# Optimization experiments

Hardware: AMD Instinct MI355X
Metric: run time of the kernel (lower is better)

Reference implementation:

```python
import jax, jax.numpy as jnp
import numpy as np

N_NODES = 50000
N_EDGES = 800000
N_FEAT = 128
N_HID = 256
N_PAIRS = 100000


def _gcn_norm(edge_index, n_nodes):
    # add self loops, compute D^-1/2 (A+I) D^-1/2 edge weights (PyG gcn_norm)
    loops = jnp.arange(n_nodes, dtype=edge_index.dtype)
    row = jnp.concatenate([edge_index[0], loops])
    col = jnp.concatenate([edge_index[1], loops])
    deg = jax.ops.segment_sum(jnp.ones_like(col, dtype=jnp.float32), col,
                              num_segments=n_nodes)
    dinv = jnp.where(deg > 0, jax.lax.rsqrt(deg), 0.0)
    norm = dinv[row] * dinv[col]  # [E + N]
    return row, col, norm


def _gcn_conv(x, W, b, row, col, norm, n_nodes):
    h = x @ W                       # [N, out]
    msg = h[row] * norm[:, None]    # gather + scale  [E+N, out]
    agg = jax.ops.segment_sum(msg, col, num_segments=n_nodes)  # scatter-add
    return agg + b


def setup_inputs() -> dict:
    key = jax.random.key(0)
    ks = jax.random.split(key, 9)
    edge_index = jax.random.randint(ks[0], (2, N_EDGES), 0, N_NODES, dtype=jnp.int64)
    features = jax.random.normal(ks[1], (N_NODES, N_FEAT), dtype=jnp.float32)
    mask = jax.random.randint(ks[2], (N_PAIRS, 2), 0, N_NODES, dtype=jnp.int64)
    s1 = 1.0 / np.sqrt(N_FEAT)
    s2 = 1.0 / np.sqrt(N_HID)
    W1 = jax.random.uniform(ks[3], (N_FEAT, N_HID), jnp.float32, -s1, s1)
    b1 = jnp.zeros((N_HID,), jnp.float32)
    W2 = jax.random.uniform(ks[4], (N_HID, N_FEAT), jnp.float32, -s2, s2)
    b2 = jnp.zeros((N_FEAT,), jnp.float32)
    Wl = jax.random.uniform(ks[5], (N_HID, 1), jnp.float32, -s2, s2)
    bl = jax.random.uniform(ks[6], (1,), jnp.float32, -s2, s2)
    return {"edge_index": edge_index, "features": features, "mask": mask,
            "W1": W1, "b1": b1, "W2": W2, "b2": b2, "Wl": Wl, "bl": bl}


def reference(edge_index, features, mask, W1, b1, W2, b2, Wl, bl):
    n = features.shape[0]
    row, col, norm = _gcn_norm(edge_index, n)
    h = _gcn_conv(features, W1, b1, row, col, norm, n)   # GCNConv a
    h = jax.nn.relu(h)                                   # dropout p=0 -> identity
    h = _gcn_conv(h, W2, b2, row, col, norm, n)          # GCNConv b
    mt = mask.T
    p1 = jax.lax.stop_gradient(h[mt[0]])                 # .detach()
    p2 = jax.lax.stop_gradient(h[mt[1]])
    hp = jnp.concatenate([p1, p2], axis=1)               # [n_pairs, 2*n_feat]
    return jax.nn.sigmoid(hp @ Wl + bl)
```

## Files before the change

### kernel.cpp

```cpp
#include <hip/hip_runtime.h>
#include <math.h>

#define NFEAT 128
#define NHID 256
#define NBLK 128

typedef __attribute__((ext_vector_type(8))) short short8;
typedef __attribute__((ext_vector_type(4))) float f32x4;

__device__ inline unsigned short f2bf(float f) {
  unsigned u = __float_as_uint(f);
  u += 0x7fffu + ((u >> 16) & 1u);
  return (unsigned short)(u >> 16);
}
__device__ inline float bflo(unsigned u) { return __uint_as_float(u << 16); }
__device__ inline float bfhi(unsigned u) { return __uint_as_float(u & 0xffff0000u); }


__device__ inline void packOne(const float* __restrict__ W,
                               unsigned short* __restrict__ Wp, int idx, int KS,
                               int OUT) {
  int lane = idx & 63;
  int t = idx >> 6;
  int ks = t % KS;
  int nt = t / KS;
  int n = nt * 16 + (lane & 15);
  int k0 = ks * 32 + (lane >> 4) * 8;
  unsigned short v[8];
#pragma unroll
  for (int j = 0; j < 8; j++) v[j] = f2bf(W[(size_t)(k0 + j) * OUT + n]);
  *reinterpret_cast<short8*>(Wp + (size_t)idx * 8) =
      *reinterpret_cast<short8*>(v);
}

__global__ __launch_bounds__(1024) void k_hist_pack(
    const int* __restrict__ col, int* __restrict__ hist2d, int nE, int nb,
    const float* __restrict__ W1, const float* __restrict__ W2,
    unsigned short* __restrict__ W1p, unsigned short* __restrict__ W2p) {
  if (blockIdx.x >= NBLK) {
    int idx = (blockIdx.x - NBLK) * 1024 + threadIdx.x;
    if (idx < 4096) packOne(W1, W1p, idx, 4, 256);
    else packOne(W2, W2p, idx - 4096, 8, 128);
    return;
  }
  __shared__ int h[1024];
  for (int i = threadIdx.x; i < nb; i += 1024) h[i] = 0;
  __syncthreads();
  int chunk = (nE + NBLK - 1) / NBLK;
  int beg = blockIdx.x * chunk, end = min(beg + chunk, nE);
  for (int e = beg + threadIdx.x; e < end; e += 1024)
    atomicAdd(&h[col[e] >> 6], 1);
  __syncthreads();
  for (int i = threadIdx.x; i < nb; i += 1024)
    hist2d[i * NBLK + blockIdx.x] = h[i];
}

__global__ __launch_bounds__(256) void k_bsum(const int* __restrict__ a,
                                              int* __restrict__ psum, int S,
                                              const float* __restrict__ b2,
                                              const float* __restrict__ Wl,
                                              const float* __restrict__ bl,
                                              float* __restrict__ Cbuf) {
  int t = threadIdx.x;
  if (blockIdx.x == gridDim.x - 1) {
    float v = (t < 128) ? b2[t] * (Wl[t] + Wl[128 + t]) : 0.f;
#pragma unroll
    for (int o = 32; o; o >>= 1) v += __shfl_down(v, o);
    __shared__ float fw[4];
    if ((t & 63) == 0) fw[t >> 6] = v;
    __syncthreads();
    if (t == 0) Cbuf[0] = fw[0] + fw[1] + fw[2] + fw[3] + bl[0];
    return;
  }
  int i = blockIdx.x * 256 + t;
  int v = (i < S) ? a[i] : 0;
#pragma unroll
  for (int o = 32; o; o >>= 1) v += __shfl_down(v, o);
  __shared__ int ws[4];
  if ((t & 63) == 0) ws[t >> 6] = v;
  __syncthreads();
  if (t == 0) psum[blockIdx.x] = ws[0] + ws[1] + ws[2] + ws[3];
}

__global__ __launch_bounds__(256) void k_s3m(const int* __restrict__ a,
                                             const int* __restrict__ psum,
                                             int* __restrict__ out, int S) {
  __shared__ int sh[256];
  __shared__ int ws[4];
  int t = threadIdx.x;
  int b = blockIdx.x;
  int partial = 0;
  for (int i = t; i < b; i += 256) partial += psum[i];
#pragma unroll
  for (int o = 32; o; o >>= 1) partial += __shfl_down(partial, o);
  if ((t & 63) == 0) ws[t >> 6] = partial;
  int i = b * 256 + t;
  int d = (i < S) ? a[i] : 0;
  sh[t] = d;
  __syncthreads();
  int base = ws[0] + ws[1] + ws[2] + ws[3];
  for (int o = 1; o < 256; o <<= 1) {
    int u = (t >= o) ? sh[t - o] : 0;
    __syncthreads();
    sh[t] += u;
    __syncthreads();
  }
  if (i < S) out[i] = base + sh[t] - d;
}

__global__ __launch_bounds__(1024) void k_part2(const int* __restrict__ row,
                                                const int* __restrict__ col,
                                                const int* __restrict__ sbase,
                                                unsigned* __restrict__ tmp,
                                                int nE, int nb) {
  __shared__ int cur[1024];
  for (int i = threadIdx.x; i < nb; i += 1024)
    cur[i] = sbase[i * NBLK + blockIdx.x];
  __syncthreads();
  int chunk = (nE + NBLK - 1) / NBLK;
  int beg = blockIdx.x * chunk, end = min(beg + chunk, nE);
  for (int e = beg + threadIdx.x; e < end; e += 1024) {
    int c = col[e];
    int pos = atomicAdd(&cur[c >> 6], 1);
    tmp[pos] = ((unsigned)(c & 63) << 16) | (unsigned)row[e];
  }
}

__global__ __launch_bounds__(256) void k_bsort_cvt(
    const unsigned* __restrict__ tmp, const int* __restrict__ sbase,
    int* __restrict__ ebuf, int* __restrict__ offs, float* __restrict__ dinv,
    const float* __restrict__ feat, unsigned short* __restrict__ xs, int n,
    int nE, int nb) {
  __shared__ int bins[64], cur[64];
  __shared__ float sdinv[64];
  int b = blockIdx.x;
  int beg = sbase[b * NBLK];
  int end = (b == nb - 1) ? nE : sbase[(b + 1) * NBLK];
  int t = threadIdx.x;
  if (t == 0 && b == nb - 1) offs[n] = nE;
  if (t < 64) bins[t] = 0;
  __syncthreads();
  for (int i = beg + t; i < end; i += 256) atomicAdd(&bins[tmp[i] >> 16], 1);
  __syncthreads();
  if (t < 64) {
    int v = bins[t];
    int s = v;
#pragma unroll
    for (int o = 1; o < 64; o <<= 1) {
      int u = __shfl_up(s, o);
      if (t >= o) s += u;
    }
    int off = beg + s - v;
    cur[t] = off;
    float dv = rsqrtf((float)(v + 1));
    sdinv[t] = dv;
    int node = b * 64 + t;
    if (node < n) {
      offs[node] = off;
      dinv[node] = dv;
    }
  }
  __syncthreads();
  for (int i = beg + t; i < end; i += 256) {
    unsigned p = tmp[i];
    int pos = atomicAdd(&cur[p >> 16], 1);
    ebuf[pos] = (int)(p & 0xffffu);
  }
  for (int i = t; i < 64 * 32; i += 256) {
    int r = i >> 5;
    int node = b * 64 + r;
    if (node >= n) break;
    float d = sdinv[r];
    float4 v = reinterpret_cast<const float4*>(feat)[(size_t)node * 32 + (i & 31)];
    unsigned short o[4] = {f2bf(v.x * d), f2bf(v.y * d), f2bf(v.z * d),
                           f2bf(v.w * d)};
    reinterpret_cast<ushort4*>(xs)[(size_t)node * 32 + (i & 31)] =
        *reinterpret_cast<ushort4*>(o);
  }
}

__global__ __launch_bounds__(256) void k_agg_bf(
    const unsigned int* __restrict__ G, const int* __restrict__ offs,
    const int* __restrict__ ebuf, const float* __restrict__ dinv,
    unsigned int* __restrict__ OUTP, int n) {
  int node = blockIdx.x * 4 + (threadIdx.x >> 6);
  if (node >= n) return;
  int lane = threadIdx.x & 63;
  int g = lane >> 4;
  int c = lane & 15;
  int beg = offs[node], end = offs[node + 1];
  float acc[8];
  if (g == 0) {
    uint4 s = *reinterpret_cast<const uint4*>(G + (size_t)node * 64 + c * 4);
    acc[0] = bflo(s.x); acc[1] = bfhi(s.x); acc[2] = bflo(s.y); acc[3] = bfhi(s.y);
    acc[4] = bflo(s.z); acc[5] = bfhi(s.z); acc[6] = bflo(s.w); acc[7] = bfhi(s.w);
  } else {
#pragma unroll
    for (int j = 0; j < 8; j++) acc[j] = 0.f;
  }
  int e = beg + g;
  for (; e + 4 < end; e += 8) {
    int i0 = ebuf[e], i1 = ebuf[e + 4];
    uint4 v0 = *reinterpret_cast<const uint4*>(G + (size_t)i0 * 64 + c * 4);
    uint4 v1 = *reinterpret_cast<const uint4*>(G + (size_t)i1 * 64 + c * 4);
    acc[0] += bflo(v0.x); acc[1] += bfhi(v0.x);
    acc[2] += bflo(v0.y); acc[3] += bfhi(v0.y);
    acc[4] += bflo(v0.z); acc[5] += bfhi(v0.z);
    acc[6] += bflo(v0.w); acc[7] += bfhi(v0.w);
    acc[0] += bflo(v1.x); acc[1] += bfhi(v1.x);
    acc[2] += bflo(v1.y); acc[3] += bfhi(v1.y);
    acc[4] += bflo(v1.z); acc[5] += bfhi(v1.z);
    acc[6] += bflo(v1.w); acc[7] += bfhi(v1.w);
  }
  if (e < end) {
    uint4 v = *reinterpret_cast<const uint4*>(G + (size_t)ebuf[e] * 64 + c * 4);
    acc[0] += bflo(v.x); acc[1] += bfhi(v.x);
    acc[2] += bflo(v.y); acc[3] += bfhi(v.y);
    acc[4] += bflo(v.z); acc[5] += bfhi(v.z);
    acc[6] += bflo(v.w); acc[7] += bfhi(v.w);
  }
#pragma unroll
  for (int j = 0; j < 8; j++) {
    acc[j] += __shfl_down(acc[j], 32);
    acc[j] += __shfl_down(acc[j], 16);
  }
  if (g == 0) {
    float d = dinv[node];
    unsigned o[4];
#pragma unroll
    for (int k = 0; k < 4; k++)
      o[k] = (unsigned)f2bf(acc[2 * k] * d) |
             ((unsigned)f2bf(acc[2 * k + 1] * d) << 16);
    *reinterpret_cast<uint4*>(OUTP + (size_t)node * 64 + c * 4) =
        *reinterpret_cast<uint4*>(o);
  }
}

__global__ __launch_bounds__(256) void k_mfma_fused(
    const unsigned short* __restrict__ A, const unsigned short* __restrict__ B1p,
    const unsigned short* __restrict__ B2p, const float* __restrict__ b1,
    const float* __restrict__ dinv, const float* __restrict__ Wl,
    float* __restrict__ P) {
  __shared__ unsigned short sh1[32 * 264];
  __shared__ float pacc[32][2];
  int rt0 = blockIdx.x * 2;
  int wave = threadIdx.x >> 6;
  int lane = threadIdx.x & 63;
  int quad = lane >> 4;
  int mrow0 = rt0 * 16 + (lane & 15);
  if (threadIdx.x < 64) pacc[threadIdx.x >> 1][threadIdx.x & 1] = 0.f;

  f32x4 acc[2][4] = {};
  const short8* Ap0 =
      reinterpret_cast<const short8*>(A + (size_t)mrow0 * NFEAT + quad * 8);
  const short8* Ap1 = reinterpret_cast<const short8*>(
      A + (size_t)(mrow0 + 16) * NFEAT + quad * 8);
#pragma unroll
  for (int ks = 0; ks < 4; ks++) {
    short8 a0 = Ap0[ks * 4];
    short8 a1 = Ap1[ks * 4];
#pragma unroll
    for (int ct = 0; ct < 4; ct++) {
      int nt = wave * 4 + ct;
      short8 b = *reinterpret_cast<const short8*>(
          B1p + ((size_t)(nt * 4 + ks) * 64 + lane) * 8);
      acc[0][ct] = __builtin_amdgcn_mfma_f32_16x16x32_bf16(a0, b, acc[0][ct], 0, 0, 0);
      acc[1][ct] = __builtin_amdgcn_mfma_f32_16x16x32_bf16(a1, b, acc[1][ct], 0, 0, 0);
    }
  }
#pragma unroll
  for (int ct = 0; ct < 4; ct++) {
    int c = (wave * 4 + ct) * 16 + (lane & 15);
    float bv = b1[c];
#pragma unroll
    for (int rg = 0; rg < 2; rg++)
#pragma unroll
      for (int i = 0; i < 4; i++) {
        float v = fmaxf(acc[rg][ct][i] + bv, 0.f);
        sh1[(rg * 16 + quad * 4 + i) * 264 + c] = f2bf(v);
      }
  }
  __syncthreads();

  f32x4 acc2[2][2] = {};
  const unsigned short* a2_0 = sh1 + (size_t)(lane & 15) * 264 + quad * 8;
  const unsigned short* a2_1 = sh1 + (size_t)(16 + (lane & 15)) * 264 + quad * 8;
#pragma unroll
  for (int ks = 0; ks < 8; ks++) {
    short8 a0 = *reinterpret_cast<const short8*>(a2_0 + ks * 32);
    short8 a1 = *reinterpret_cast<const short8*>(a2_1 + ks * 32);
#pragma unroll
    for (int ct = 0; ct < 2; ct++) {
      int nt = wave * 2 + ct;
      short8 b = *reinterpret_cast<const short8*>(
          B2p + ((size_t)(nt * 8 + ks) * 64 + lane) * 8);
      acc2[0][ct] = __builtin_amdgcn_mfma_f32_16x16x32_bf16(a0, b, acc2[0][ct], 0, 0, 0);
      acc2[1][ct] = __builtin_amdgcn_mfma_f32_16x16x32_bf16(a1, b, acc2[1][ct], 0, 0, 0);
    }
  }
  float p1[2][4] = {}, p2[2][4] = {};
#pragma unroll
  for (int rg = 0; rg < 2; rg++) {
    int r0 = (rt0 + rg) * 16 + quad * 4;
    float dv[4];
#pragma unroll
    for (int i = 0; i < 4; i++) dv[i] = dinv[r0 + i];
#pragma unroll
    for (int ct = 0; ct < 2; ct++) {
      int c = (wave * 2 + ct) * 16 + (lane & 15);
      float wl1 = Wl[c], wl2 = Wl[128 + c];
#pragma unroll
      for (int i = 0; i < 4; i++) {
        float v = acc2[rg][ct][i] * dv[i];
        p1[rg][i] = fmaf(v, wl1, p1[rg][i]);
        p2[rg][i] = fmaf(v, wl2, p2[rg][i]);
      }
    }
  }
#pragma unroll
  for (int rg = 0; rg < 2; rg++)
#pragma unroll
    for (int i = 0; i < 4; i++) {
#pragma unroll
      for (int o = 8; o; o >>= 1) {
        p1[rg][i] += __shfl_xor(p1[rg][i], o);
        p2[rg][i] += __shfl_xor(p2[rg][i], o);
      }
    }
  if ((lane & 15) == 0) {
#pragma unroll
    for (int rg = 0; rg < 2; rg++)
#pragma unroll
      for (int i = 0; i < 4; i++) {
        int row = rg * 16 + quad * 4 + i;
        atomicAdd(&pacc[row][0], p1[rg][i]);
        atomicAdd(&pacc[row][1], p2[rg][i]);
      }
  }
  __syncthreads();
  if (threadIdx.x < 64) {
    int row = threadIdx.x >> 1, comp = threadIdx.x & 1;
    P[(size_t)(rt0 * 16 + row) * 2 + comp] = pacc[row][comp];
  }
}

__global__ __launch_bounds__(256) void k_agg_s(const float2* __restrict__ p,
                                               const int* __restrict__ offs,
                                               const int* __restrict__ ebuf,
                                               const float* __restrict__ dinv,
                                               float2* __restrict__ q, int n) {
  int i = blockIdx.x * 256 + threadIdx.x;
  if (i >= n) return;
  int beg = offs[i], end = offs[i + 1];
  float2 s = p[i];
  int e = beg;
  for (; e + 4 <= end; e += 4) {
    int s0 = ebuf[e], s1 = ebuf[e + 1], s2 = ebuf[e + 2], s3 = ebuf[e + 3];
    float2 v0 = p[s0], v1 = p[s1], v2 = p[s2], v3 = p[s3];
    s.x += v0.x + v1.x + v2.x + v3.x;
    s.y += v0.y + v1.y + v2.y + v3.y;
  }
  for (; e < end; e++) {
    float2 v = p[ebuf[e]];
    s.x += v.x;
    s.y += v.y;
  }
  float d = dinv[i];
  q[i] = make_float2(s.x * d, s.y * d);
}

__global__ __launch_bounds__(256) void k_head2(const float2* __restrict__ q,
                                               const int* __restrict__ mask,
                                               const float* __restrict__ Cbuf,
                                               float* __restrict__ out, int P) {
  int p = blockIdx.x * 256 + threadIdx.x;
  if (p >= P) return;
  int m0 = mask[2 * p], m1 = mask[2 * p + 1];
  float s = q[m0].x + q[m1].y + Cbuf[0];
  out[p] = 1.0f / (1.0f + expf(-s));
}

extern "C" void kernel_launch(void* const* d_in, const int* in_sizes, int n_in,
                              void* d_out, int out_size, void* d_ws,
                              size_t ws_size, hipStream_t stream) {
  const int* edge = (const int*)d_in[0];
  const float* feat = (const float*)d_in[1];
  const int* mask = (const int*)d_in[2];
  const float* W1 = (const float*)d_in[3];
  const float* b1 = (const float*)d_in[4];
  const float* W2 = (const float*)d_in[5];
  const float* b2 = (const float*)d_in[6];
  const float* Wl = (const float*)d_in[7];
  const float* bl = (const float*)d_in[8];
  float* out = (float*)d_out;

  const int E = in_sizes[0] / 2;
  const int N = in_sizes[1] / NFEAT;
  const int P = in_sizes[2] / 2;
  const int* rowp = edge;
  const int* colp = edge + E;
  const int nrt = N / 16;
  const int nb = (N + 63) / 64;
  const int S = nb * NBLK;
  const int nS = (S + 255) / 256;

  auto aln = [](size_t x) { return (x + 255) & ~(size_t)255; };
  const size_t rowSlack = (size_t)16 * NFEAT * 2;
  char* w = (char*)d_ws;
  int* hist2d = (int*)w;           w += aln((size_t)S * 4);
  int* sbase = (int*)w;            w += aln((size_t)S * 4);
  int* psum = (int*)w;             w += aln((size_t)1024 * 4);
  float* Cbuf = (float*)w;         w += aln(256);
  int* offs = (int*)w;             w += aln((size_t)(N + 1) * 4);
  int* ebuf = (int*)w;             w += aln((size_t)E * 4);
  unsigned* tmp = (unsigned*)w;    w += aln((size_t)E * 4);
  float* dinv = (float*)w;         w += aln((size_t)N * 4 + 1024);
  unsigned short* xs = (unsigned short*)w;  w += aln((size_t)N * NFEAT * 2);
  unsigned short* z = (unsigned short*)w;   w += aln((size_t)N * NFEAT * 2 + rowSlack);
  float* p = (float*)w;            w += aln((size_t)(N + 32) * 8);
  float2* q = (float2*)w;          w += aln((size_t)N * 8);
  unsigned short* W1p = (unsigned short*)w; w += aln((size_t)NFEAT * NHID * 2);
  unsigned short* W2p = (unsigned short*)w; w += aln((size_t)NHID * NFEAT * 2);

  k_hist_pack<<<NBLK + 8, 1024, 0, stream>>>(colp, hist2d, E, nb, W1, W2, W1p,
                                             W2p);
  k_bsum<<<nS + 1, 256, 0, stream>>>(hist2d, psum, S, b2, Wl, bl, Cbuf);
  k_s3m<<<nS, 256, 0, stream>>>(hist2d, psum, sbase, S);
  k_part2<<<NBLK, 1024, 0, stream>>>(rowp, colp, sbase, tmp, E, nb);
  k_bsort_cvt<<<nb, 256, 0, stream>>>(tmp, sbase, ebuf, offs, dinv, feat, xs,
                                      N, E, nb);
  k_agg_bf<<<(N + 3) / 4, 256, 0, stream>>>((const unsigned*)xs, offs, ebuf,
                                            dinv, (unsigned*)z, N);
  k_mfma_fused<<<(nrt + 1) / 2, 256, 0, stream>>>(z, W1p, W2p, b1, dinv, Wl, p);
  k_agg_s<<<(N + 255) / 256, 256, 0, stream>>>((const float2*)p, offs, ebuf,
                                               dinv, q, N);
  k_head2<<<(P + 255) / 256, 256, 0, stream>>>(q, mask, Cbuf, out, P);
}
```

Measured before the change: 173.9 us.

## Fuse graph-build kernels into one persistent kernel with global barriers

```diff
diff --git a/kernel.cpp b/kernel.cpp
--- a/kernel.cpp
+++ b/kernel.cpp
@@ -15,7 +15,6 @@
 }
 __device__ inline float bflo(unsigned u) { return __uint_as_float(u << 16); }
 __device__ inline float bfhi(unsigned u) { return __uint_as_float(u & 0xffff0000u); }
-
 
 __device__ inline void packOne(const float* __restrict__ W,
                                unsigned short* __restrict__ Wp, int idx, int KS,
@@ -33,149 +32,169 @@
       *reinterpret_cast<short8*>(v);
 }
 
-__global__ __launch_bounds__(1024) void k_hist_pack(
-    const int* __restrict__ col, int* __restrict__ hist2d, int nE, int nb,
-    const float* __restrict__ W1, const float* __restrict__ W2,
-    unsigned short* __restrict__ W1p, unsigned short* __restrict__ W2p) {
-  if (blockIdx.x >= NBLK) {
-    int idx = (blockIdx.x - NBLK) * 1024 + threadIdx.x;
-    if (idx < 4096) packOne(W1, W1p, idx, 4, 256);
-    else packOne(W2, W2p, idx - 4096, 8, 128);
-    return;
-  }
-  __shared__ int h[1024];
-  for (int i = threadIdx.x; i < nb; i += 1024) h[i] = 0;
-  __syncthreads();
-  int chunk = (nE + NBLK - 1) / NBLK;
-  int beg = blockIdx.x * chunk, end = min(beg + chunk, nE);
-  for (int e = beg + threadIdx.x; e < end; e += 1024)
-    atomicAdd(&h[col[e] >> 6], 1);
-  __syncthreads();
-  for (int i = threadIdx.x; i < nb; i += 1024)
-    hist2d[i * NBLK + blockIdx.x] = h[i];
-}
-
-__global__ __launch_bounds__(256) void k_bsum(const int* __restrict__ a,
-                                              int* __restrict__ psum, int S,
-                                              const float* __restrict__ b2,
-                                              const float* __restrict__ Wl,
-                                              const float* __restrict__ bl,
-                                              float* __restrict__ Cbuf) {
-  int t = threadIdx.x;
-  if (blockIdx.x == gridDim.x - 1) {
-    float v = (t < 128) ? b2[t] * (Wl[t] + Wl[128 + t]) : 0.f;
+__device__ inline void gbar(int* cnt, int target) {
+  __syncthreads();
+  if (threadIdx.x == 0) {
+    __threadfence();
+    atomicAdd(cnt, 1);
+    while (atomicAdd(cnt, 0) < target) __builtin_amdgcn_s_sleep(8);
+  }
+  __syncthreads();
+}
+
+struct BuildParams {
+  const int* row;
+  const int* col;
+  int* bar;
+  int* hist2d;
+  int* psum;
+  int* sbase;
+  unsigned* tmp;
+  int* ebuf;
+  int* offs;
+  float* dinv;
+  const float* feat;
+  unsigned short* xs;
+  const float* W1;
+  const float* W2;
+  unsigned short* W1p;
+  unsigned short* W2p;
+  const float* b2;
+  const float* Wl;
+  const float* bl;
+  float* Cbuf;
+  int E, N, nb;
+};
+
+__global__ __launch_bounds__(1024) void k_build(BuildParams P) {
+  __shared__ int sA[1024];
+  __shared__ int sB[1024];
+  const int b = blockIdx.x;
+  const int t = threadIdx.x;
+  const int nb = P.nb;
+  const int chunk = (P.E + NBLK - 1) / NBLK;
+  const int ebeg = b * chunk, eend = min(ebeg + chunk, P.E);
+
+  for (int i = t; i < nb; i += 1024) sA[i] = 0;
+  __syncthreads();
+  for (int e = ebeg + t; e < eend; e += 1024) atomicAdd(&sA[P.col[e] >> 6], 1);
+  __syncthreads();
+  for (int i = t; i < nb; i += 1024) P.hist2d[i * NBLK + b] = sA[i];
+  if (b < 8) {
+    int idx = b * 1024 + t;
+    if (idx < 4096) packOne(P.W1, P.W1p, idx, 4, 256);
+    else packOne(P.W2, P.W2p, idx - 4096, 8, 128);
+  }
+  if (b == 8) {
+    float v = (t < 128) ? P.b2[t] * (P.Wl[t] + P.Wl[128 + t]) : 0.f;
 #pragma unroll
     for (int o = 32; o; o >>= 1) v += __shfl_down(v, o);
-    __shared__ float fw[4];
-    if ((t & 63) == 0) fw[t >> 6] = v;
-    __syncthreads();
-    if (t == 0) Cbuf[0] = fw[0] + fw[1] + fw[2] + fw[3] + bl[0];
-    return;
-  }
-  int i = blockIdx.x * 256 + t;
-  int v = (i < S) ? a[i] : 0;
-#pragma unroll
-  for (int o = 32; o; o >>= 1) v += __shfl_down(v, o);
-  __shared__ int ws[4];
-  if ((t & 63) == 0) ws[t >> 6] = v;
-  __syncthreads();
-  if (t == 0) psum[blockIdx.x] = ws[0] + ws[1] + ws[2] + ws[3];
-}
-
-__global__ __launch_bounds__(256) void k_s3m(const int* __restrict__ a,
-                                             const int* __restrict__ psum,
-                                             int* __restrict__ out, int S) {
-  __shared__ int sh[256];
-  __shared__ int ws[4];
-  int t = threadIdx.x;
-  int b = blockIdx.x;
-  int partial = 0;
-  for (int i = t; i < b; i += 256) partial += psum[i];
-#pragma unroll
-  for (int o = 32; o; o >>= 1) partial += __shfl_down(partial, o);
-  if ((t & 63) == 0) ws[t >> 6] = partial;
-  int i = b * 256 + t;
-  int d = (i < S) ? a[i] : 0;
-  sh[t] = d;
-  __syncthreads();
-  int base = ws[0] + ws[1] + ws[2] + ws[3];
-  for (int o = 1; o < 256; o <<= 1) {
-    int u = (t >= o) ? sh[t - o] : 0;
-    __syncthreads();
-    sh[t] += u;
-    __syncthreads();
-  }
-  if (i < S) out[i] = base + sh[t] - d;
-}
-
-__global__ __launch_bounds__(1024) void k_part2(const int* __restrict__ row,
-                                                const int* __restrict__ col,
-                                                const int* __restrict__ sbase,
-                                                unsigned* __restrict__ tmp,
-                                                int nE, int nb) {
-  __shared__ int cur[1024];
-  for (int i = threadIdx.x; i < nb; i += 1024)
-    cur[i] = sbase[i * NBLK + blockIdx.x];
-  __syncthreads();
-  int chunk = (nE + NBLK - 1) / NBLK;
-  int beg = blockIdx.x * chunk, end = min(beg + chunk, nE);
-  for (int e = beg + threadIdx.x; e < end; e += 1024) {
-    int c = col[e];
-    int pos = atomicAdd(&cur[c >> 6], 1);
-    tmp[pos] = ((unsigned)(c & 63) << 16) | (unsigned)row[e];
-  }
-}
-
-__global__ __launch_bounds__(256) void k_bsort_cvt(
-    const unsigned* __restrict__ tmp, const int* __restrict__ sbase,
-    int* __restrict__ ebuf, int* __restrict__ offs, float* __restrict__ dinv,
-    const float* __restrict__ feat, unsigned short* __restrict__ xs, int n,
-    int nE, int nb) {
-  __shared__ int bins[64], cur[64];
-  __shared__ float sdinv[64];
-  int b = blockIdx.x;
-  int beg = sbase[b * NBLK];
-  int end = (b == nb - 1) ? nE : sbase[(b + 1) * NBLK];
-  int t = threadIdx.x;
-  if (t == 0 && b == nb - 1) offs[n] = nE;
-  if (t < 64) bins[t] = 0;
-  __syncthreads();
-  for (int i = beg + t; i < end; i += 256) atomicAdd(&bins[tmp[i] >> 16], 1);
-  __syncthreads();
-  if (t < 64) {
-    int v = bins[t];
-    int s = v;
-#pragma unroll
-    for (int o = 1; o < 64; o <<= 1) {
-      int u = __shfl_up(s, o);
-      if (t >= o) s += u;
-    }
-    int off = beg + s - v;
-    cur[t] = off;
-    float dv = rsqrtf((float)(v + 1));
-    sdinv[t] = dv;
-    int node = b * 64 + t;
-    if (node < n) {
-      offs[node] = off;
-      dinv[node] = dv;
-    }
-  }
-  __syncthreads();
-  for (int i = beg + t; i < end; i += 256) {
-    unsigned p = tmp[i];
-    int pos = atomicAdd(&cur[p >> 16], 1);
-    ebuf[pos] = (int)(p & 0xffffu);
-  }
-  for (int i = t; i < 64 * 32; i += 256) {
-    int r = i >> 5;
-    int node = b * 64 + r;
-    if (node >= n) break;
-    float d = sdinv[r];
-    float4 v = reinterpret_cast<const float4*>(feat)[(size_t)node * 32 + (i & 31)];
-    unsigned short o[4] = {f2bf(v.x * d), f2bf(v.y * d), f2bf(v.z * d),
-                           f2bf(v.w * d)};
-    reinterpret_cast<ushort4*>(xs)[(size_t)node * 32 + (i & 31)] =
-        *reinterpret_cast<ushort4*>(o);
+    if ((t & 63) == 0) ((float*)sB)[t >> 6] = v;
+    __syncthreads();
+    if (t == 0) {
+      float s = 0.f;
+      for (int w2 = 0; w2 < 16; w2++) s += ((float*)sB)[w2];
+      P.Cbuf[0] = s + P.bl[0];
+    }
+  }
+  gbar(P.bar + 0, NBLK);
+
+  const int S = nb * NBLK;
+  const int perb = (S + NBLK - 1) / NBLK;
+  const int s0 = b * perb, s1 = min(s0 + perb, S);
+  {
+    int v = 0;
+    for (int i = s0 + t; i < s1; i += 1024) v += P.hist2d[i];
+#pragma unroll
+    for (int o = 32; o; o >>= 1) v += __shfl_down(v, o);
+    if ((t & 63) == 0) sA[t >> 6] = v;
+    __syncthreads();
+    if (t == 0) {
+      int s = 0;
+      for (int w2 = 0; w2 < 16; w2++) s += sA[w2];
+      P.psum[b] = s;
+    }
+  }
+  gbar(P.bar + 1, NBLK);
+
+  {
+    int v = (t < b) ? P.psum[t] : 0;
+#pragma unroll
+    for (int o = 32; o; o >>= 1) v += __shfl_down(v, o);
+    if ((t & 63) == 0) sA[t >> 6] = v;
+    __syncthreads();
+    int base = 0;
+    for (int w2 = 0; w2 < 16; w2++) base += sA[w2];
+    int n1 = s1 - s0;
+    int d = (t < n1) ? P.hist2d[s0 + t] : 0;
+    sB[t] = d;
+    __syncthreads();
+    for (int o = 1; o < 1024; o <<= 1) {
+      int u = (t >= o) ? sB[t - o] : 0;
+      __syncthreads();
+      sB[t] += u;
+      __syncthreads();
+    }
+    if (t < n1) P.sbase[s0 + t] = base + sB[t] - d;
+  }
+  gbar(P.bar + 2, NBLK);
+
+  {
+    for (int i = t; i < nb; i += 1024) sA[i] = P.sbase[i * NBLK + b];
+    __syncthreads();
+    for (int e = ebeg + t; e < eend; e += 1024) {
+      int c = P.col[e];
+      int pos = atomicAdd(&sA[c >> 6], 1);
+      P.tmp[pos] = ((unsigned)(c & 63) << 16) | (unsigned)P.row[e];
+    }
+  }
+  gbar(P.bar + 3, NBLK);
+
+  if (t == 0 && b == 0) P.offs[P.N] = P.E;
+  for (int bkt = b; bkt < nb; bkt += NBLK) {
+    __syncthreads();
+    if (t < 64) sA[t] = 0;
+    __syncthreads();
+    int e0 = P.sbase[bkt * NBLK];
+    int e1 = (bkt == nb - 1) ? P.E : P.sbase[(bkt + 1) * NBLK];
+    for (int i = e0 + t; i < e1; i += 1024) atomicAdd(&sA[P.tmp[i] >> 16], 1);
+    __syncthreads();
+    if (t < 64) {
+      int v = sA[t];
+      int s = v;
+#pragma unroll
+      for (int o = 1; o < 64; o <<= 1) {
+        int u = __shfl_up(s, o);
+        if (t >= o) s += u;
+      }
+      int off = e0 + s - v;
+      sB[t] = off;
+      float dv = rsqrtf((float)(v + 1));
+      ((float*)sA)[64 + t] = dv;
+      int node = bkt * 64 + t;
+      if (node < P.N) {
+        P.offs[node] = off;
+        P.dinv[node] = dv;
+      }
+    }
+    __syncthreads();
+    for (int i = e0 + t; i < e1; i += 1024) {
+      unsigned p = P.tmp[i];
+      int pos = atomicAdd(&sB[p >> 16], 1);
+      P.ebuf[pos] = (int)(p & 0xffffu);
+    }
+    for (int i = t; i < 64 * 32; i += 1024) {
+      int r = i >> 5;
+      int node = bkt * 64 + r;
+      if (node >= P.N) break;
+      float d = ((float*)sA)[64 + r];
+      float4 v =
+          reinterpret_cast<const float4*>(P.feat)[(size_t)node * 32 + (i & 31)];
+      unsigned short o[4] = {f2bf(v.x * d), f2bf(v.y * d), f2bf(v.z * d),
+                             f2bf(v.w * d)};
+      reinterpret_cast<ushort4*>(P.xs)[(size_t)node * 32 + (i & 31)] =
+          *reinterpret_cast<ushort4*>(o);
+    }
   }
 }
 
@@ -402,11 +421,11 @@
   const int nrt = N / 16;
   const int nb = (N + 63) / 64;
   const int S = nb * NBLK;
-  const int nS = (S + 255) / 256;
 
   auto aln = [](size_t x) { return (x + 255) & ~(size_t)255; };
   const size_t rowSlack = (size_t)16 * NFEAT * 2;
   char* w = (char*)d_ws;
+  int* bars = (int*)w;             w += aln(256);
   int* hist2d = (int*)w;           w += aln((size_t)S * 4);
   int* sbase = (int*)w;            w += aln((size_t)S * 4);
   int* psum = (int*)w;             w += aln((size_t)1024 * 4);
@@ -422,13 +441,18 @@
   unsigned short* W1p = (unsigned short*)w; w += aln((size_t)NFEAT * NHID * 2);
   unsigned short* W2p = (unsigned short*)w; w += aln((size_t)NHID * NFEAT * 2);
 
-  k_hist_pack<<<NBLK + 8, 1024, 0, stream>>>(colp, hist2d, E, nb, W1, W2, W1p,
-                                             W2p);
-  k_bsum<<<nS + 1, 256, 0, stream>>>(hist2d, psum, S, b2, Wl, bl, Cbuf);
-  k_s3m<<<nS, 256, 0, stream>>>(hist2d, psum, sbase, S);
-  k_part2<<<NBLK, 1024, 0, stream>>>(rowp, colp, sbase, tmp, E, nb);
-  k_bsort_cvt<<<nb, 256, 0, stream>>>(tmp, sbase, ebuf, offs, dinv, feat, xs,
-                                      N, E, nb);
+  hipMemsetAsync(bars, 0, 256, stream);
+
+  BuildParams bp;
+  bp.row = rowp; bp.col = colp; bp.bar = bars;
+  bp.hist2d = hist2d; bp.psum = psum; bp.sbase = sbase;
+  bp.tmp = tmp; bp.ebuf = ebuf; bp.offs = offs; bp.dinv = dinv;
+  bp.feat = feat; bp.xs = xs;
+  bp.W1 = W1; bp.W2 = W2; bp.W1p = W1p; bp.W2p = W2p;
+  bp.b2 = b2; bp.Wl = Wl; bp.bl = bl; bp.Cbuf = Cbuf;
+  bp.E = E; bp.N = N; bp.nb = nb;
+  k_build<<<NBLK, 1024, 0, stream>>>(bp);
+
   k_agg_bf<<<(N + 3) / 4, 256, 0, stream>>>((const unsigned*)xs, offs, ebuf,
                                             dinv, (unsigned*)z, N);
   k_mfma_fused<<<(nrt + 1) / 2, 256, 0, stream>>>(z, W1p, W2p, b1, dinv, Wl, p);
```

Result: slower. 215.9 us (+24.1%).
